# Performance work log

Hardware: AMD Instinct MI355X
Metric: run time of the kernel (lower is better)

## Reference

```python
import jax, jax.numpy as jnp
import numpy as np

B, NX, NY = 16, 1024, 1024


def _grad(f, axis):
    # torch.gradient(f, dim=axis, edge_order=2), unit spacing
    fm = jnp.moveaxis(f, axis, -1)
    g = (jnp.roll(fm, -1, -1) - jnp.roll(fm, 1, -1)) * 0.5
    g0 = (-3.0 * fm[..., 0] + 4.0 * fm[..., 1] - fm[..., 2]) * 0.5
    gN = (3.0 * fm[..., -1] - 4.0 * fm[..., -2] + fm[..., -3]) * 0.5
    g = g.at[..., 0].set(g0).at[..., -1].set(gN)
    return jnp.moveaxis(g, -1, axis)


def _grad2(f, axis):
    # roll-based second derivative with one-sided 2nd-order boundary stencils
    fm = jnp.moveaxis(f, axis, -1)
    g = jnp.roll(fm, -1, -1) - 2.0 * fm + jnp.roll(fm, 1, -1)
    g0 = 2.0 * fm[..., 0] - 5.0 * fm[..., 1] + 4.0 * fm[..., 2] - fm[..., 3]
    gN = 2.0 * fm[..., -1] - 5.0 * fm[..., -2] + 4.0 * fm[..., -3] - fm[..., -4]
    g = g.at[..., 0].set(g0).at[..., -1].set(gN)
    return jnp.moveaxis(g, -1, axis)


def setup_inputs() -> dict:
    key = jax.random.key(0)
    k1, k2, k3, k4 = jax.random.split(key, 4)
    f = jax.random.uniform(k1, (B, NX, NY), dtype=jnp.float32)
    A_grid = jax.random.normal(k2, (2, NX, NY), dtype=jnp.float32)
    B_grid = jax.random.uniform(k3, (3, NX, NY), dtype=jnp.float32)
    dt = jax.random.uniform(k4, (B,), dtype=jnp.float32)
    return {"f": f, "A_grid": A_grid, "B_grid": B_grid, "dt": dt}


def reference(f, A_grid, B_grid, dt):
    # Af: [B,2,NX,NY], Bf: [B,3,NX,NY]
    Af = A_grid[None] * f[:, None]
    Bf = B_grid[None] * f[:, None]
    gradv_Af = _grad(Af[:, 0], 1) + _grad(Af[:, 1], 2)
    gradvv_Bf = (
        _grad2(Bf[:, 0], 1)
        + _grad2(Bf[:, 1], 2)
        + _grad(_grad(Bf[:, 2], 2), 1)
        + _grad(_grad(Bf[:, 2], 1), 2)
    )
    df = -gradv_Af + gradvv_Bf * 0.5
    f_new = f + df * dt[:, None, None]
    # ensure_non_negative_f=True
    return jnp.maximum(f_new, 0.0)
```

## Files before the change

### kernel.cpp

```cpp
#include <hip/hip_runtime.h>

#define BATCH 16
#define NX 1024
#define NY 1024
#define CHUNK 16
#define PLANE (NX * NY)

struct Row4 {
    float fc[4];
    float pa[4];
    float rr[4];
    float dq[4];
    float d2s[4];
    float dtT[4];
};

__device__ __forceinline__ Row4 make_row4(
    int xx, int y0, int tid,
    const float* __restrict__ fb, const float* __restrict__ A0,
    const float* __restrict__ A1, const float* __restrict__ B0,
    const float* __restrict__ B1, const float* __restrict__ B2)
{
    const int base = xx * NY + y0;
    const bool has_l = (tid > 0);
    const bool has_r = (tid < 255);

    const float4 f4 = *(const float4*)(fb + base);
    const float fl = has_l ? fb[base - 1] : 0.0f;
    const float fr = has_r ? fb[base + 4] : 0.0f;

    const float4 a0 = *(const float4*)(A0 + base);
    const float4 b0 = *(const float4*)(B0 + base);

    const float4 a1 = *(const float4*)(A1 + base);
    const float a1l = has_l ? A1[base - 1] : 0.0f;
    const float a1r = has_r ? A1[base + 4] : 0.0f;

    const float4 b1 = *(const float4*)(B1 + base);
    const float b1l = has_l ? B1[base - 1] : 0.0f;
    const float b1r = has_r ? B1[base + 4] : 0.0f;

    const float4 b2 = *(const float4*)(B2 + base);
    const float b2l = has_l ? B2[base - 1] : 0.0f;
    const float b2r = has_r ? B2[base + 4] : 0.0f;

    float fe[6] = { fl, f4.x, f4.y, f4.z, f4.w, fr };
    float qe[6] = { a1l * fl, a1.x * f4.x, a1.y * f4.y, a1.z * f4.z, a1.w * f4.w, a1r * fr };
    float se[6] = { b1l * fl, b1.x * f4.x, b1.y * f4.y, b1.z * f4.z, b1.w * f4.w, b1r * fr };
    float te[6] = { b2l * fl, b2.x * f4.x, b2.y * f4.y, b2.z * f4.z, b2.w * f4.w, b2r * fr };

    Row4 r;
    r.fc[0] = fe[1]; r.fc[1] = fe[2]; r.fc[2] = fe[3]; r.fc[3] = fe[4];
    r.pa[0] = a0.x * f4.x; r.pa[1] = a0.y * f4.y; r.pa[2] = a0.z * f4.z; r.pa[3] = a0.w * f4.w;
    r.rr[0] = b0.x * f4.x; r.rr[1] = b0.y * f4.y; r.rr[2] = b0.z * f4.z; r.rr[3] = b0.w * f4.w;

    #pragma unroll
    for (int i = 0; i < 4; ++i) {
        r.dq[i]  = 0.5f * (qe[i + 2] - qe[i]);
        r.d2s[i] = se[i + 2] - 2.0f * se[i + 1] + se[i];
        r.dtT[i] = 0.5f * (te[i + 2] - te[i]);
    }
    if (tid == 0) {
        r.dq[0]  = 0.5f * (-3.0f * qe[1] + 4.0f * qe[2] - qe[3]);
        r.d2s[0] = 2.0f * se[1] - 5.0f * se[2] + 4.0f * se[3] - se[4];
        r.dtT[0] = 0.5f * (-3.0f * te[1] + 4.0f * te[2] - te[3]);
    }
    if (tid == 255) {
        r.dq[3]  = 0.5f * (3.0f * qe[4] - 4.0f * qe[3] + qe[2]);
        r.d2s[3] = 2.0f * se[4] - 5.0f * se[3] + 4.0f * se[2] - se[1];
        r.dtT[3] = 0.5f * (3.0f * te[4] - 4.0f * te[3] + te[2]);
    }
    return r;
}

__global__ __launch_bounds__(256) void fp2d_kernel(
    const float* __restrict__ f,
    const float* __restrict__ Ag,
    const float* __restrict__ Bg,
    const float* __restrict__ dt,
    float* __restrict__ out)
{
    const int tid = threadIdx.x;
    const int y0  = tid * 4;
    const int x0  = blockIdx.x * CHUNK;
    const int b   = blockIdx.y;

    const float* __restrict__ fb = f + (size_t)b * PLANE;
    float* __restrict__ ob = out + (size_t)b * PLANE;
    const float dtb = dt[b];
    const float* __restrict__ A0 = Ag;
    const float* __restrict__ A1 = Ag + PLANE;
    const float* __restrict__ B0 = Bg;
    const float* __restrict__ B1 = Bg + PLANE;
    const float* __restrict__ B2 = Bg + 2 * PLANE;

    int cs = x0;
    int ce = x0 + CHUNK - 1;
    if (cs == 0) cs = 1;
    if (ce == NX - 1) ce = NX - 2;

    Row4 m = make_row4(cs - 1, y0, tid, fb, A0, A1, B0, B1, B2);
    Row4 c = make_row4(cs,     y0, tid, fb, A0, A1, B0, B1, B2);
    #pragma unroll 2
    for (int x = cs; x <= ce; ++x) {
        Row4 p = make_row4(x + 1, y0, tid, fb, A0, A1, B0, B1, B2);
        float4 o;
        float* op = &o.x;
        #pragma unroll
        for (int i = 0; i < 4; ++i) {
            const float dxP   = 0.5f * (p.pa[i] - m.pa[i]);
            const float dxxR  = p.rr[i] - 2.0f * c.rr[i] + m.rr[i];
            const float dxdyT = 0.5f * (p.dtT[i] - m.dtT[i]);
            const float df = -(dxP + c.dq[i]) + 0.5f * (dxxR + c.d2s[i]) + dxdyT;
            op[i] = fmaxf(c.fc[i] + df * dtb, 0.0f);
        }
        *(float4*)(ob + x * NY + y0) = o;
        m = c; c = p;
    }

    if (x0 == 0) {
        Row4 r0 = make_row4(0, y0, tid, fb, A0, A1, B0, B1, B2);
        Row4 r1 = make_row4(1, y0, tid, fb, A0, A1, B0, B1, B2);
        Row4 r2 = make_row4(2, y0, tid, fb, A0, A1, B0, B1, B2);
        Row4 r3 = make_row4(3, y0, tid, fb, A0, A1, B0, B1, B2);
        float4 o; float* op = &o.x;
        #pragma unroll
        for (int i = 0; i < 4; ++i) {
            const float dxP   = 0.5f * (-3.0f * r0.pa[i] + 4.0f * r1.pa[i] - r2.pa[i]);
            const float dxxR  = 2.0f * r0.rr[i] - 5.0f * r1.rr[i] + 4.0f * r2.rr[i] - r3.rr[i];
            const float dxdyT = 0.5f * (-3.0f * r0.dtT[i] + 4.0f * r1.dtT[i] - r2.dtT[i]);
            const float df = -(dxP + r0.dq[i]) + 0.5f * (dxxR + r0.d2s[i]) + dxdyT;
            op[i] = fmaxf(r0.fc[i] + df * dtb, 0.0f);
        }
        *(float4*)(ob + y0) = o;
    }

    if (x0 + CHUNK == NX) {
        Row4 r0 = make_row4(NX - 1, y0, tid, fb, A0, A1, B0, B1, B2);
        Row4 r1 = make_row4(NX - 2, y0, tid, fb, A0, A1, B0, B1, B2);
        Row4 r2 = make_row4(NX - 3, y0, tid, fb, A0, A1, B0, B1, B2);
        Row4 r3 = make_row4(NX - 4, y0, tid, fb, A0, A1, B0, B1, B2);
        float4 o; float* op = &o.x;
        #pragma unroll
        for (int i = 0; i < 4; ++i) {
            const float dxP   = 0.5f * (3.0f * r0.pa[i] - 4.0f * r1.pa[i] + r2.pa[i]);
            const float dxxR  = 2.0f * r0.rr[i] - 5.0f * r1.rr[i] + 4.0f * r2.rr[i] - r3.rr[i];
            const float dxdyT = 0.5f * (3.0f * r0.dtT[i] - 4.0f * r1.dtT[i] + r2.dtT[i]);
            const float df = -(dxP + r0.dq[i]) + 0.5f * (dxxR + r0.d2s[i]) + dxdyT;
            op[i] = fmaxf(r0.fc[i] + df * dtb, 0.0f);
        }
        *(float4*)(ob + (NX - 1) * NY + y0) = o;
    }
}

extern "C" void kernel_launch(void* const* d_in, const int* in_sizes, int n_in,
                              void* d_out, int out_size, void* d_ws, size_t ws_size,
                              hipStream_t stream) {
    const float* f  = (const float*)d_in[0];
    const float* Ag = (const float*)d_in[1];
    const float* Bg = (const float*)d_in[2];
    const float* dt = (const float*)d_in[3];
    float* out = (float*)d_out;

    dim3 block(256, 1, 1);
    dim3 grid(NX / CHUNK, BATCH, 1);
    fp2d_kernel<<<grid, block, 0, stream>>>(f, Ag, Bg, dt, out);
}
```

Baseline: 170.3 us.

## Prefetch next row, share halos via wave shuffles, use nontemporal stores

The row loads are split from the arithmetic so that the loads for row x+2 are issued while row x is computed. This gives register-level software pipelining. Neighbour values in y now come from cross-lane shuffles, so only wave-edge lanes issue the scalar halo loads instead of every thread loading eight extra scalars. Output stores use nontemporal hints to avoid polluting cache. The cost is higher register pressure from holding a raw row in flight, plus the shuffle instructions.

```diff
diff --git a/kernel.cpp b/kernel.cpp
--- a/kernel.cpp
+++ b/kernel.cpp
@@ -6,71 +6,89 @@
 #define CHUNK 16
 #define PLANE (NX * NY)
 
-struct Row4 {
-    float fc[4];
-    float pa[4];
-    float rr[4];
-    float dq[4];
-    float d2s[4];
-    float dtT[4];
+typedef float v4f __attribute__((ext_vector_type(4)));
+
+
+struct Raw {
+    v4f f, a0, a1, b0, b1, b2;
+    float fl, a1l, b1l, b2l;
+    float fr, a1r, b1r, b2r;
 };
 
-__device__ __forceinline__ Row4 make_row4(
-    int xx, int y0, int tid,
+struct Row4 { float fc[4], pa[4], rr[4], dq[4], d2s[4], dtT[4]; };
+
+__device__ __forceinline__ Raw load_raw(int xx, int y0, int tid,
     const float* __restrict__ fb, const float* __restrict__ A0,
     const float* __restrict__ A1, const float* __restrict__ B0,
     const float* __restrict__ B1, const float* __restrict__ B2)
 {
     const int base = xx * NY + y0;
-    const bool has_l = (tid > 0);
-    const bool has_r = (tid < 255);
+    Raw r;
+    r.f  = *(const v4f*)(fb + base);
+    r.a0 = *(const v4f*)(A0 + base);
+    r.a1 = *(const v4f*)(A1 + base);
+    r.b0 = *(const v4f*)(B0 + base);
+    r.b1 = *(const v4f*)(B1 + base);
+    r.b2 = *(const v4f*)(B2 + base);
 
-    const float4 f4 = *(const float4*)(fb + base);
-    const float fl = has_l ? fb[base - 1] : 0.0f;
-    const float fr = has_r ? fb[base + 4] : 0.0f;
+    const int lane = tid & 63;
+    const bool nl = (lane == 0)  && (tid > 0);
+    const bool nr = (lane == 63) && (tid < 255);
+    r.fl  = nl ? fb[base - 1] : 0.0f;
+    r.a1l = nl ? A1[base - 1] : 0.0f;
+    r.b1l = nl ? B1[base - 1] : 0.0f;
+    r.b2l = nl ? B2[base - 1] : 0.0f;
+    r.fr  = nr ? fb[base + 4] : 0.0f;
+    r.a1r = nr ? A1[base + 4] : 0.0f;
+    r.b1r = nr ? B1[base + 4] : 0.0f;
+    r.b2r = nr ? B2[base + 4] : 0.0f;
+    return r;
+}
 
-    const float4 a0 = *(const float4*)(A0 + base);
-    const float4 b0 = *(const float4*)(B0 + base);
+__device__ __forceinline__ Row4 convert(const Raw& r, int tid)
+{
+    const int lane = tid & 63;
 
-    const float4 a1 = *(const float4*)(A1 + base);
-    const float a1l = has_l ? A1[base - 1] : 0.0f;
-    const float a1r = has_r ? A1[base + 4] : 0.0f;
+    const float q0 = r.a1.x * r.f.x, q1 = r.a1.y * r.f.y,
+                q2 = r.a1.z * r.f.z, q3 = r.a1.w * r.f.w;
+    const float s0 = r.b1.x * r.f.x, s1 = r.b1.y * r.f.y,
+                s2 = r.b1.z * r.f.z, s3 = r.b1.w * r.f.w;
+    const float t0 = r.b2.x * r.f.x, t1 = r.b2.y * r.f.y,
+                t2 = r.b2.z * r.f.z, t3 = r.b2.w * r.f.w;
 
-    const float4 b1 = *(const float4*)(B1 + base);
-    const float b1l = has_l ? B1[base - 1] : 0.0f;
-    const float b1r = has_r ? B1[base + 4] : 0.0f;
+    float qm = __shfl_up(q3, 1), sm = __shfl_up(s3, 1), tm = __shfl_up(t3, 1);
+    float qp = __shfl_down(q0, 1), sp = __shfl_down(s0, 1), tp = __shfl_down(t0, 1);
+    if (lane == 0)  { qm = r.a1l * r.fl; sm = r.b1l * r.fl; tm = r.b2l * r.fl; }
+    if (lane == 63) { qp = r.a1r * r.fr; sp = r.b1r * r.fr; tp = r.b2r * r.fr; }
 
-    const float4 b2 = *(const float4*)(B2 + base);
-    const float b2l = has_l ? B2[base - 1] : 0.0f;
-    const float b2r = has_r ? B2[base + 4] : 0.0f;
+    const float qe[6] = { qm, q0, q1, q2, q3, qp };
+    const float se[6] = { sm, s0, s1, s2, s3, sp };
+    const float te[6] = { tm, t0, t1, t2, t3, tp };
 
-    float fe[6] = { fl, f4.x, f4.y, f4.z, f4.w, fr };
-    float qe[6] = { a1l * fl, a1.x * f4.x, a1.y * f4.y, a1.z * f4.z, a1.w * f4.w, a1r * fr };
-    float se[6] = { b1l * fl, b1.x * f4.x, b1.y * f4.y, b1.z * f4.z, b1.w * f4.w, b1r * fr };
-    float te[6] = { b2l * fl, b2.x * f4.x, b2.y * f4.y, b2.z * f4.z, b2.w * f4.w, b2r * fr };
-
-    Row4 r;
-    r.fc[0] = fe[1]; r.fc[1] = fe[2]; r.fc[2] = fe[3]; r.fc[3] = fe[4];
-    r.pa[0] = a0.x * f4.x; r.pa[1] = a0.y * f4.y; r.pa[2] = a0.z * f4.z; r.pa[3] = a0.w * f4.w;
-    r.rr[0] = b0.x * f4.x; r.rr[1] = b0.y * f4.y; r.rr[2] = b0.z * f4.z; r.rr[3] = b0.w * f4.w;
+    Row4 o;
+    o.fc[0] = r.f.x; o.fc[1] = r.f.y; o.fc[2] = r.f.z; o.fc[3] = r.f.w;
+    o.pa[0] = r.a0.x * r.f.x; o.pa[1] = r.a0.y * r.f.y;
+    o.pa[2] = r.a0.z * r.f.z; o.pa[3] = r.a0.w * r.f.w;
+    o.rr[0] = r.b0.x * r.f.x; o.rr[1] = r.b0.y * r.f.y;
+    o.rr[2] = r.b0.z * r.f.z; o.rr[3] = r.b0.w * r.f.w;
 
     #pragma unroll
     for (int i = 0; i < 4; ++i) {
-        r.dq[i]  = 0.5f * (qe[i + 2] - qe[i]);
-        r.d2s[i] = se[i + 2] - 2.0f * se[i + 1] + se[i];
-        r.dtT[i] = 0.5f * (te[i + 2] - te[i]);
+        o.dq[i]  = 0.5f * (qe[i + 2] - qe[i]);
+        o.d2s[i] = se[i + 2] - 2.0f * se[i + 1] + se[i];
+        o.dtT[i] = 0.5f * (te[i + 2] - te[i]);
     }
     if (tid == 0) {
-        r.dq[0]  = 0.5f * (-3.0f * qe[1] + 4.0f * qe[2] - qe[3]);
-        r.d2s[0] = 2.0f * se[1] - 5.0f * se[2] + 4.0f * se[3] - se[4];
-        r.dtT[0] = 0.5f * (-3.0f * te[1] + 4.0f * te[2] - te[3]);
+        o.dq[0]  = 0.5f * (-3.0f * qe[1] + 4.0f * qe[2] - qe[3]);
+        o.d2s[0] = 2.0f * se[1] - 5.0f * se[2] + 4.0f * se[3] - se[4];
+        o.dtT[0] = 0.5f * (-3.0f * te[1] + 4.0f * te[2] - te[3]);
     }
     if (tid == 255) {
-        r.dq[3]  = 0.5f * (3.0f * qe[4] - 4.0f * qe[3] + qe[2]);
-        r.d2s[3] = 2.0f * se[4] - 5.0f * se[3] + 4.0f * se[2] - se[1];
-        r.dtT[3] = 0.5f * (3.0f * te[4] - 4.0f * te[3] + te[2]);
+        o.dq[3]  = 0.5f * (3.0f * qe[4] - 4.0f * qe[3] + qe[2]);
+        o.d2s[3] = 2.0f * se[4] - 5.0f * se[3] + 4.0f * se[2] - se[1];
+        o.dtT[3] = 0.5f * (3.0f * te[4] - 4.0f * te[3] + te[2]);
     }
-    return r;
+    return o;
 }
 
 __global__ __launch_bounds__(256) void fp2d_kernel(
@@ -94,62 +112,63 @@
     const float* __restrict__ B1 = Bg + PLANE;
     const float* __restrict__ B2 = Bg + 2 * PLANE;
 
-    int cs = x0;
-    int ce = x0 + CHUNK - 1;
-    if (cs == 0) cs = 1;
-    if (ce == NX - 1) ce = NX - 2;
+    const int cs = (x0 == 0) ? 1 : x0;
+    const int ce = (x0 + CHUNK == NX) ? NX - 2 : x0 + CHUNK - 1;
 
-    Row4 m = make_row4(cs - 1, y0, tid, fb, A0, A1, B0, B1, B2);
-    Row4 c = make_row4(cs,     y0, tid, fb, A0, A1, B0, B1, B2);
+    Row4 m = convert(load_raw(cs - 1, y0, tid, fb, A0, A1, B0, B1, B2), tid);
+    Row4 c = convert(load_raw(cs,     y0, tid, fb, A0, A1, B0, B1, B2), tid);
+    Raw rp = load_raw(cs + 1, y0, tid, fb, A0, A1, B0, B1, B2);
+
     #pragma unroll 2
     for (int x = cs; x <= ce; ++x) {
-        Row4 p = make_row4(x + 1, y0, tid, fb, A0, A1, B0, B1, B2);
-        float4 o;
-        float* op = &o.x;
+        const int xn = (x + 2 < NX) ? x + 2 : NX - 1;
+        Raw rn = load_raw(xn, y0, tid, fb, A0, A1, B0, B1, B2);
+        Row4 p = convert(rp, tid);
+        v4f o;
         #pragma unroll
         for (int i = 0; i < 4; ++i) {
             const float dxP   = 0.5f * (p.pa[i] - m.pa[i]);
             const float dxxR  = p.rr[i] - 2.0f * c.rr[i] + m.rr[i];
             const float dxdyT = 0.5f * (p.dtT[i] - m.dtT[i]);
             const float df = -(dxP + c.dq[i]) + 0.5f * (dxxR + c.d2s[i]) + dxdyT;
-            op[i] = fmaxf(c.fc[i] + df * dtb, 0.0f);
+            o[i] = fmaxf(c.fc[i] + df * dtb, 0.0f);
         }
-        *(float4*)(ob + x * NY + y0) = o;
-        m = c; c = p;
+        __builtin_nontemporal_store(o, (v4f*)(ob + x * NY + y0));
+        m = c; c = p; rp = rn;
     }
 
     if (x0 == 0) {
-        Row4 r0 = make_row4(0, y0, tid, fb, A0, A1, B0, B1, B2);
-        Row4 r1 = make_row4(1, y0, tid, fb, A0, A1, B0, B1, B2);
-        Row4 r2 = make_row4(2, y0, tid, fb, A0, A1, B0, B1, B2);
-        Row4 r3 = make_row4(3, y0, tid, fb, A0, A1, B0, B1, B2);
-        float4 o; float* op = &o.x;
+        Row4 r0 = convert(load_raw(0, y0, tid, fb, A0, A1, B0, B1, B2), tid);
+        Row4 r1 = convert(load_raw(1, y0, tid, fb, A0, A1, B0, B1, B2), tid);
+        Row4 r2 = convert(load_raw(2, y0, tid, fb, A0, A1, B0, B1, B2), tid);
+        Row4 r3 = convert(load_raw(3, y0, tid, fb, A0, A1, B0, B1, B2), tid);
+        v4f o;
         #pragma unroll
         for (int i = 0; i < 4; ++i) {
             const float dxP   = 0.5f * (-3.0f * r0.pa[i] + 4.0f * r1.pa[i] - r2.pa[i]);
             const float dxxR  = 2.0f * r0.rr[i] - 5.0f * r1.rr[i] + 4.0f * r2.rr[i] - r3.rr[i];
             const float dxdyT = 0.5f * (-3.0f * r0.dtT[i] + 4.0f * r1.dtT[i] - r2.dtT[i]);
             const float df = -(dxP + r0.dq[i]) + 0.5f * (dxxR + r0.d2s[i]) + dxdyT;
-            op[i] = fmaxf(r0.fc[i] + df * dtb, 0.0f);
+            o[i] = fmaxf(r0.fc[i] + df * dtb, 0.0f);
         }
-        *(float4*)(ob + y0) = o;
+        __builtin_nontemporal_store(o, (v4f*)(ob + y0));
     }
 
     if (x0 + CHUNK == NX) {
-        Row4 r0 = make_row4(NX - 1, y0, tid, fb, A0, A1, B0, B1, B2);
-        Row4 r1 = make_row4(NX - 2, y0, tid, fb, A0, A1, B0, B1, B2);
-        Row4 r2 = make_row4(NX - 3, y0, tid, fb, A0, A1, B0, B1, B2);
-        Row4 r3 = make_row4(NX - 4, y0, tid, fb, A0, A1, B0, B1, B2);
-        float4 o; float* op = &o.x;
+        Row4 r0 = convert(load_raw(NX - 1, y0, tid, fb, A0, A1, B0, B1, B2), tid);
+        Row4 r1 = convert(load_raw(NX - 2, y0, tid, fb, A0, A1, B0, B1, B2), tid);
+        Row4 r2 = convert(load_raw(NX - 3, y0, tid, fb, A0, A1, B0, B1, B2), tid);
+        Row4 r3 = convert(load_raw(NX - 4, y0, tid, fb, A0, A1, B0, B1, B2), tid);
+        v4f o;
         #pragma unroll
         for (int i = 0; i < 4; ++i) {
             const float dxP   = 0.5f * (3.0f * r0.pa[i] - 4.0f * r1.pa[i] + r2.pa[i]);
             const float dxxR  = 2.0f * r0.rr[i] - 5.0f * r1.rr[i] + 4.0f * r2.rr[i] - r3.rr[i];
             const float dxdyT = 0.5f * (3.0f * r0.dtT[i] - 4.0f * r1.dtT[i] + r2.dtT[i]);
             const float df = -(dxP + r0.dq[i]) + 0.5f * (dxxR + r0.d2s[i]) + dxdyT;
-            op[i] = fmaxf(r0.fc[i] + df * dtb, 0.0f);
+            o[i] = fmaxf(r0.fc[i] + df * dtb, 0.0f);
         }
-        *(float4*)(ob + (NX - 1) * NY + y0) = o;
+        __builtin_nontemporal_store(o, (v4f*)(ob + (NX - 1) * NY + y0));
     }
 }
 
```

Measured after the change: 161.7 us. 1.05x faster.
